# Performance work log

Measured on AMD Instinct MI355X. Metric: run time of the kernel, lower is better.

## Reference

```python
import jax, jax.numpy as jnp
import numpy as np

N_NODES = 50000


def gcn_conv(x, W, b, src, dst, n):
    """PyG GCNConv: add self-loops, symmetric deg^-1/2 normalization, then aggregate."""
    loop = jnp.arange(n, dtype=src.dtype)
    s = jnp.concatenate([src, loop])  # [E+N]
    d = jnp.concatenate([dst, loop])  # [E+N]
    deg = jax.ops.segment_sum(jnp.ones_like(d, dtype=x.dtype), d, num_segments=n)  # [N]
    dinv = jnp.where(deg > 0, jax.lax.rsqrt(deg), 0.0)
    h = x @ W  # transform first (reduces message width), [N, out]
    norm = (dinv[s] * dinv[d])[:, None]  # [E+N, 1]
    msgs = h[s] * norm  # gather + scale, [E+N, out]
    out = jax.ops.segment_sum(msgs, d, num_segments=n)  # scatter-add, [N, out]
    return out + b


def setup_inputs() -> dict:
    key = jax.random.key(0)
    k1, k2, k3, k4 = jax.random.split(key, 4)
    in_dim, hidden, n_cls = 512, 256, 64
    x = jax.random.normal(k1, (N_NODES, in_dim), dtype=jnp.float32)
    edge_index = jax.random.randint(k2, (2, 800000), 0, N_NODES, dtype=jnp.int64)
    W1 = jax.random.normal(k3, (in_dim, hidden), dtype=jnp.float32) / np.sqrt(in_dim)
    b1 = jnp.zeros((hidden,), dtype=jnp.float32)
    W2 = jax.random.normal(k4, (hidden, n_cls), dtype=jnp.float32) / np.sqrt(hidden)
    b2 = jnp.zeros((n_cls,), dtype=jnp.float32)
    return {"x": x, "edge_index": edge_index, "W1": W1, "b1": b1, "W2": W2, "b2": b2}


def reference(x, edge_index, W1, b1, W2, b2):
    src, dst = edge_index[0], edge_index[1]
    n = x.shape[0]
    h = jax.nn.relu(gcn_conv(x, W1, b1, src, dst, n))  # dropout is identity in eval mode
    logits = gcn_conv(h, W2, b2, src, dst, n)
    evidence = jax.nn.softplus(logits)
    return (evidence, h)
```

## Files before the change

### kernel.cpp

```cpp
#include <hip/hip_runtime.h>


#define N_NODES 50000
#define IN_DIM 512
#define HID 256
#define NCLS 64

typedef unsigned short u16;
typedef unsigned int u32;
typedef __attribute__((ext_vector_type(8))) short short8;
typedef __attribute__((ext_vector_type(4))) float float4_t;

__device__ __forceinline__ float bf_lo(u32 v) {
    u32 u = v << 16; float f; __builtin_memcpy(&f, &u, 4); return f;
}
__device__ __forceinline__ float bf_hi(u32 v) {
    u32 u = v & 0xffff0000u; float f; __builtin_memcpy(&f, &u, 4); return f;
}
__device__ __forceinline__ u16 f2bf(float f) {
    u32 u; __builtin_memcpy(&u, &f, 4);
    return (u16)((u + 0x7fffu + ((u >> 16) & 1u)) >> 16);
}
__device__ __forceinline__ void acc8(float* acc, uint4 v, float w) {
    acc[0] += w * bf_lo(v.x); acc[1] += w * bf_hi(v.x);
    acc[2] += w * bf_lo(v.y); acc[3] += w * bf_hi(v.y);
    acc[4] += w * bf_lo(v.z); acc[5] += w * bf_hi(v.z);
    acc[6] += w * bf_lo(v.w); acc[7] += w * bf_hi(v.w);
}

__global__ void init_kernel(int* __restrict__ cnt, int* __restrict__ cursor, int n) {
    int i = blockIdx.x * blockDim.x + threadIdx.x;
    if (i < n) { cnt[i] = 0; cursor[i] = 0; }
}

__global__ void count_kernel(const int* __restrict__ dst, int* __restrict__ cnt, int E) {
    int e = blockIdx.x * blockDim.x + threadIdx.x;
    if (e < E) atomicAdd(&cnt[dst[e]], 1);
}

__global__ __launch_bounds__(256) void s1_kernel(const int* __restrict__ cnt,
                                                 int* __restrict__ blocksum,
                                                 float* __restrict__ dinv, int n) {
    int tid = threadIdx.x;
    int i = blockIdx.x * 256 + tid;
    int c = (i < n) ? cnt[i] : 0;
    if (i < n) dinv[i] = rsqrtf((float)(c + 1));
    __shared__ int s[256];
    s[tid] = c;
    __syncthreads();
    for (int off = 128; off > 0; off >>= 1) {
        if (tid < off) s[tid] += s[tid + off];
        __syncthreads();
    }
    if (tid == 0) blocksum[blockIdx.x] = s[0];
}

__global__ __launch_bounds__(256) void s3_kernel(const int* __restrict__ cnt,
                                                 const int* __restrict__ blocksum,
                                                 int* __restrict__ row_ptr, int n, int nb) {
    __shared__ int bs[256];
    __shared__ int s[256];
    int tid = threadIdx.x;
    int v = (tid < nb) ? blocksum[tid] : 0;
    bs[tid] = v;
    __syncthreads();
    for (int off = 1; off < 256; off <<= 1) {
        int a = (tid >= off) ? bs[tid - off] : 0;
        __syncthreads();
        bs[tid] += a;
        __syncthreads();
    }
    int boff = (blockIdx.x == 0) ? 0 : bs[blockIdx.x - 1];
    int i = blockIdx.x * 256 + tid;
    int c = (i < n) ? cnt[i] : 0;
    s[tid] = c;
    __syncthreads();
    for (int off = 1; off < 256; off <<= 1) {
        int a = (tid >= off) ? s[tid - off] : 0;
        __syncthreads();
        s[tid] += a;
        __syncthreads();
    }
    if (i <= n) row_ptr[i] = boff + s[tid] - c;
}

__global__ void fill_kernel(const int* __restrict__ src, const int* __restrict__ dst,
                            const int* __restrict__ row_ptr, int* __restrict__ cursor,
                            int* __restrict__ csr_src, int E) {
    int e = blockIdx.x * blockDim.x + threadIdx.x;
    if (e >= E) return;
    int d = dst[e];
    int pos = row_ptr[d] + atomicAdd(&cursor[d], 1);
    csr_src[pos] = src[e];
}

__global__ __launch_bounds__(256) void cast_bf16_kernel(const float* __restrict__ in,
                                                        u16* __restrict__ out, int n4) {
    int i = blockIdx.x * 256 + threadIdx.x;
    if (i >= n4) return;
    float4 v = ((const float4*)in)[i];
    ushort4 o = make_ushort4(f2bf(v.x), f2bf(v.y), f2bf(v.z), f2bf(v.w));
    ((ushort4*)out)[i] = o;
}

__global__ __launch_bounds__(256) void tcast_kernel(const float* __restrict__ W,
                                                    u16* __restrict__ Wt, int K, int N) {
    int idx = blockIdx.x * 256 + threadIdx.x;
    if (idx >= K * N) return;
    int n = idx / K, k = idx - n * K;
    Wt[idx] = f2bf(W[k * N + n]);
}

template <int BM, int BN, int K, int N>
__global__ __launch_bounds__(256) void mfma_gemm_kernel(const u16* __restrict__ A,
                                                        const u16* __restrict__ Bt,
                                                        u16* __restrict__ C, int M) {
    constexpr int WCOLS = (BN >= 128) ? 2 : 1;
    constexpr int WROWS = 4 / WCOLS;
    static_assert(WROWS * 64 == BM && WCOLS * 64 == BN, "wave tiling mismatch");
    constexpr int LDSA = BM * 32;
    __shared__ u16 lds[LDSA + BN * 32];

    const int tid = threadIdx.x;
    const int wave = tid >> 6, lane = tid & 63;
    const int wm = wave / WCOLS, wn = wave % WCOLS;
    const int quad = lane >> 4, l15 = lane & 15;
    const int row0 = blockIdx.y * BM;
    const int col0 = blockIdx.x * BN;

    float4_t acc[4][4];
#pragma unroll
    for (int mi = 0; mi < 4; mi++)
#pragma unroll
        for (int ni = 0; ni < 4; ni++) {
            float4_t z = {0.f, 0.f, 0.f, 0.f};
            acc[mi][ni] = z;
        }

    for (int k0 = 0; k0 < K; k0 += 32) {
#pragma unroll
        for (int i = 0; i < BM / 64; i++) {
            int c = tid + i * 256;
            int r = c >> 2;
            int gr = row0 + r;
            gr = gr < M ? gr : M - 1;
            const u16* gp = A + (long)gr * K + k0 + (c & 3) * 8;
            u16* lp = lds + c * 8;
            __builtin_amdgcn_global_load_lds((const __attribute__((address_space(1))) u32*)gp,
                                             (__attribute__((address_space(3))) u32*)lp,
                                             16, 0, 0);
        }
#pragma unroll
        for (int i = 0; i < BN / 64; i++) {
            int c = tid + i * 256;
            int r = c >> 2;
            const u16* gp = Bt + (long)(col0 + r) * K + k0 + (c & 3) * 8;
            u16* lp = lds + LDSA + c * 8;
            __builtin_amdgcn_global_load_lds((const __attribute__((address_space(1))) u32*)gp,
                                             (__attribute__((address_space(3))) u32*)lp,
                                             16, 0, 0);
        }
        __syncthreads();

        short8 af[4], bfr[4];
#pragma unroll
        for (int mi = 0; mi < 4; mi++)
            af[mi] = *(const short8*)(lds + (wm * 64 + mi * 16 + l15) * 32 + quad * 8);
#pragma unroll
        for (int ni = 0; ni < 4; ni++)
            bfr[ni] = *(const short8*)(lds + LDSA + (wn * 64 + ni * 16 + l15) * 32 + quad * 8);
#pragma unroll
        for (int mi = 0; mi < 4; mi++)
#pragma unroll
            for (int ni = 0; ni < 4; ni++)
                acc[mi][ni] = __builtin_amdgcn_mfma_f32_16x16x32_bf16(af[mi], bfr[ni],
                                                                      acc[mi][ni], 0, 0, 0);
        __syncthreads();
    }

#pragma unroll
    for (int mi = 0; mi < 4; mi++) {
#pragma unroll
        for (int r = 0; r < 4; r++) {
            int row = row0 + wm * 64 + mi * 16 + quad * 4 + r;
            if (row < M) {
#pragma unroll
                for (int ni = 0; ni < 4; ni++) {
                    int col = col0 + wn * 64 + ni * 16 + l15;
                    C[(long)row * N + col] = f2bf(acc[mi][ni][r]);
                }
            }
        }
    }
}

__global__ __launch_bounds__(256) void agg_wide_kernel(const u16* __restrict__ t,
                                                       const int* __restrict__ row_ptr,
                                                       const int* __restrict__ csr_src,
                                                       const float* __restrict__ dinv,
                                                       const float* __restrict__ bias,
                                                       float* __restrict__ out_f,
                                                       u16* __restrict__ out_bf, int n) {
    constexpr int FEAT = 256;
    int node = (blockIdx.x * blockDim.x + threadIdx.x) >> 6;
    int lane = threadIdx.x & 63;
    if (node >= n) return;
    const int g = lane >> 5;
    const int r = lane & 31;
    float acc[8] = {};
    const int beg = row_ptr[node], end = row_ptr[node + 1];
    int e = beg;
    for (; e + 16 <= end; e += 16) {
        int s[8]; float w[8]; uint4 v[8];
#pragma unroll
        for (int u = 0; u < 8; u++) s[u] = csr_src[e + u * 2 + g];
#pragma unroll
        for (int u = 0; u < 8; u++) w[u] = dinv[s[u]];
#pragma unroll
        for (int u = 0; u < 8; u++) v[u] = *(const uint4*)(t + (long)s[u] * FEAT + r * 8);
#pragma unroll
        for (int u = 0; u < 8; u++) acc8(acc, v[u], w[u]);
    }
    for (; e + 8 <= end; e += 8) {
        int s[4]; float w[4]; uint4 v[4];
#pragma unroll
        for (int u = 0; u < 4; u++) s[u] = csr_src[e + u * 2 + g];
#pragma unroll
        for (int u = 0; u < 4; u++) w[u] = dinv[s[u]];
#pragma unroll
        for (int u = 0; u < 4; u++) v[u] = *(const uint4*)(t + (long)s[u] * FEAT + r * 8);
#pragma unroll
        for (int u = 0; u < 4; u++) acc8(acc, v[u], w[u]);
    }
    for (; e < end; e += 2) {
        int ee = e + g;
        if (ee < end) {
            int s = csr_src[ee];
            float w = dinv[s];
            uint4 v = *(const uint4*)(t + (long)s * FEAT + r * 8);
            acc8(acc, v, w);
        }
    }
#pragma unroll
    for (int j = 0; j < 8; j++) acc[j] += __shfl_xor(acc[j], 32, 64);

    if (lane < 32) {
        const float di = dinv[node];
        uint4 sv = *(const uint4*)(t + (long)node * FEAT + lane * 8);
        float self[8] = {bf_lo(sv.x), bf_hi(sv.x), bf_lo(sv.y), bf_hi(sv.y),
                         bf_lo(sv.z), bf_hi(sv.z), bf_lo(sv.w), bf_hi(sv.w)};
        float4 b0 = *(const float4*)(bias + lane * 8);
        float4 b1 = *(const float4*)(bias + lane * 8 + 4);
        float bb[8] = {b0.x, b0.y, b0.z, b0.w, b1.x, b1.y, b1.z, b1.w};
        float rv[8];
#pragma unroll
        for (int j = 0; j < 8; j++)
            rv[j] = fmaxf(di * (acc[j] + di * self[j]) + bb[j], 0.f);
        long base = (long)node * FEAT + lane * 8;
        *(float4*)(out_f + base) = make_float4(rv[0], rv[1], rv[2], rv[3]);
        *(float4*)(out_f + base + 4) = make_float4(rv[4], rv[5], rv[6], rv[7]);
        uint4 o;
        o.x = (u32)f2bf(rv[0]) | ((u32)f2bf(rv[1]) << 16);
        o.y = (u32)f2bf(rv[2]) | ((u32)f2bf(rv[3]) << 16);
        o.z = (u32)f2bf(rv[4]) | ((u32)f2bf(rv[5]) << 16);
        o.w = (u32)f2bf(rv[6]) | ((u32)f2bf(rv[7]) << 16);
        *(uint4*)(out_bf + base) = o;
    }
}

__global__ __launch_bounds__(256) void agg_n8_kernel(const u16* __restrict__ t,
                                                     const int* __restrict__ row_ptr,
                                                     const int* __restrict__ csr_src,
                                                     const float* __restrict__ dinv,
                                                     const float* __restrict__ bias,
                                                     float* __restrict__ out_f, int n) {
    constexpr int FEAT = 64;
    const int wid = (blockIdx.x * blockDim.x + threadIdx.x) >> 6;
    const int lane = threadIdx.x & 63;
    const int g = lane >> 3;
    const int r = lane & 7;
    const int node = wid * 8 + g;
    const bool valid = node < n;
    const int nd = valid ? node : (n - 1);
    const int beg = row_ptr[nd];
    const int deg = valid ? (row_ptr[nd + 1] - beg) : 0;
    float acc[8] = {};
    for (int e = 0;; e += 4) {
        if (!__any(e < deg)) break;
        int s[4]; float w[4]; uint4 v[4];
#pragma unroll
        for (int u = 0; u < 4; u++) {
            bool a = (e + u) < deg;
            s[u] = a ? csr_src[beg + e + u] : 0;
            w[u] = a ? 0.f : 0.f;
            w[u] = a ? 1.f : 0.f;
        }
#pragma unroll
        for (int u = 0; u < 4; u++) w[u] = w[u] * dinv[s[u]];
#pragma unroll
        for (int u = 0; u < 4; u++) v[u] = *(const uint4*)(t + (long)s[u] * FEAT + r * 8);
#pragma unroll
        for (int u = 0; u < 4; u++) acc8(acc, v[u], w[u]);
    }
    const float di = dinv[nd];
    uint4 sv = *(const uint4*)(t + (long)nd * FEAT + r * 8);
    float self[8] = {bf_lo(sv.x), bf_hi(sv.x), bf_lo(sv.y), bf_hi(sv.y),
                     bf_lo(sv.z), bf_hi(sv.z), bf_lo(sv.w), bf_hi(sv.w)};
    float4 b0 = *(const float4*)(bias + r * 8);
    float4 b1 = *(const float4*)(bias + r * 8 + 4);
    float bb[8] = {b0.x, b0.y, b0.z, b0.w, b1.x, b1.y, b1.z, b1.w};
    float rv[8];
#pragma unroll
    for (int j = 0; j < 8; j++) {
        float v = di * (acc[j] + di * self[j]) + bb[j];
        rv[j] = fmaxf(v, 0.f) + __logf(1.f + __expf(-fabsf(v)));
    }
    if (valid) {
        long base = (long)nd * FEAT + r * 8;
        *(float4*)(out_f + base) = make_float4(rv[0], rv[1], rv[2], rv[3]);
        *(float4*)(out_f + base + 4) = make_float4(rv[4], rv[5], rv[6], rv[7]);
    }
}

extern "C" void kernel_launch(void* const* d_in, const int* in_sizes, int n_in,
                              void* d_out, int out_size, void* d_ws, size_t ws_size,
                              hipStream_t stream) {
    const float* x  = (const float*)d_in[0];
    const int*   ei = (const int*)d_in[1];
    const float* W1 = (const float*)d_in[2];
    const float* b1 = (const float*)d_in[3];
    const float* W2 = (const float*)d_in[4];
    const float* b2 = (const float*)d_in[5];

    float* evidence = (float*)d_out;
    float* h        = (float*)d_out + (long)N_NODES * NCLS;

    const int E = in_sizes[1] / 2;
    const int* src = ei;
    const int* dst = ei + E;

    const int NB = (N_NODES + 255) / 256;

    char* w = (char*)d_ws;
    int*   cnt      = (int*)w;  w += 50048 * 4;
    int*   cursor   = (int*)w;  w += 50048 * 4;
    int*   row_ptr  = (int*)w;  w += 50064 * 4;
    float* dinv     = (float*)w; w += 50048 * 4;
    int*   blocksum = (int*)w;  w += 256 * 4;
    int*   csr_src  = (int*)w;  w += 800000 * 4;
    u16*   xbf      = (u16*)w;  w += (long)N_NODES * IN_DIM * 2;
    u16*   w1t      = (u16*)w;  w += IN_DIM * HID * 2;
    u16*   w2t      = (u16*)w;  w += HID * NCLS * 2;
    u16*   t1bf     = (u16*)w;  w += (long)N_NODES * HID * 2;
    u16*   hbf      = xbf;
    u16*   t2bf     = t1bf;

    init_kernel<<<NB, 256, 0, stream>>>(cnt, cursor, N_NODES);
    count_kernel<<<(E + 255) / 256, 256, 0, stream>>>(dst, cnt, E);
    s1_kernel<<<NB, 256, 0, stream>>>(cnt, blocksum, dinv, N_NODES);
    s3_kernel<<<NB, 256, 0, stream>>>(cnt, blocksum, row_ptr, N_NODES, NB);
    fill_kernel<<<(E + 255) / 256, 256, 0, stream>>>(src, dst, row_ptr, cursor, csr_src, E);

    cast_bf16_kernel<<<(N_NODES * IN_DIM / 4 + 255) / 256, 256, 0, stream>>>(
        x, xbf, N_NODES * IN_DIM / 4);
    tcast_kernel<<<(IN_DIM * HID + 255) / 256, 256, 0, stream>>>(W1, w1t, IN_DIM, HID);
    tcast_kernel<<<(HID * NCLS + 255) / 256, 256, 0, stream>>>(W2, w2t, HID, NCLS);

    {
        dim3 grid(HID / 128, (N_NODES + 127) / 128);
        mfma_gemm_kernel<128, 128, IN_DIM, HID><<<grid, 256, 0, stream>>>(xbf, w1t, t1bf, N_NODES);
    }
    agg_wide_kernel<<<(N_NODES * 64 + 255) / 256, 256, 0, stream>>>(
        t1bf, row_ptr, csr_src, dinv, b1, h, hbf, N_NODES);

    {
        dim3 grid(NCLS / 64, (N_NODES + 255) / 256);
        mfma_gemm_kernel<256, 64, HID, NCLS><<<grid, 256, 0, stream>>>(hbf, w2t, t2bf, N_NODES);
    }
    {
        int waves = (N_NODES + 7) / 8;
        int blocks = (waves + 3) / 4;
        agg_n8_kernel<<<blocks, 256, 0, stream>>>(
            t2bf, row_ptr, csr_src, dinv, b2, evidence, N_NODES);
    }
}
```

Before: 410.7 us.

## Fuse fp32-to-bf16 cast into GEMM A-load and prescale rows by dinv

Drops the separate x-to-bf16 cast kernel; the first GEMM now reads fp32 x directly and converts it to bf16 while staging into LDS. Both GEMMs multiply output rows by dinv in the epilogue, so the aggregation kernels no longer gather dinv per neighbour and just sum the rows. This avoids writing and re-reading a bf16 copy of x and removes one random gather per edge. In exchange, the first GEMM reads twice the bytes through a register path instead of the direct global-to-LDS load, and dinv is applied before the bf16 rounding.

```diff
diff --git a/kernel.cpp b/kernel.cpp
--- a/kernel.cpp
+++ b/kernel.cpp
@@ -20,6 +20,12 @@
 __device__ __forceinline__ u16 f2bf(float f) {
     u32 u; __builtin_memcpy(&u, &f, 4);
     return (u16)((u + 0x7fffu + ((u >> 16) & 1u)) >> 16);
+}
+__device__ __forceinline__ void add8(float* acc, uint4 v) {
+    acc[0] += bf_lo(v.x); acc[1] += bf_hi(v.x);
+    acc[2] += bf_lo(v.y); acc[3] += bf_hi(v.y);
+    acc[4] += bf_lo(v.z); acc[5] += bf_hi(v.z);
+    acc[6] += bf_lo(v.w); acc[7] += bf_hi(v.w);
 }
 __device__ __forceinline__ void acc8(float* acc, uint4 v, float w) {
     acc[0] += w * bf_lo(v.x); acc[1] += w * bf_hi(v.x);
@@ -94,15 +100,6 @@
     csr_src[pos] = src[e];
 }
 
-__global__ __launch_bounds__(256) void cast_bf16_kernel(const float* __restrict__ in,
-                                                        u16* __restrict__ out, int n4) {
-    int i = blockIdx.x * 256 + threadIdx.x;
-    if (i >= n4) return;
-    float4 v = ((const float4*)in)[i];
-    ushort4 o = make_ushort4(f2bf(v.x), f2bf(v.y), f2bf(v.z), f2bf(v.w));
-    ((ushort4*)out)[i] = o;
-}
-
 __global__ __launch_bounds__(256) void tcast_kernel(const float* __restrict__ W,
                                                     u16* __restrict__ Wt, int K, int N) {
     int idx = blockIdx.x * 256 + threadIdx.x;
@@ -111,10 +108,11 @@
     Wt[idx] = f2bf(W[k * N + n]);
 }
 
-template <int BM, int BN, int K, int N>
-__global__ __launch_bounds__(256) void mfma_gemm_kernel(const u16* __restrict__ A,
+template <int BM, int BN, int K, int N, bool AF32, bool SCALE>
+__global__ __launch_bounds__(256) void mfma_gemm_kernel(const void* __restrict__ Ain,
                                                         const u16* __restrict__ Bt,
-                                                        u16* __restrict__ C, int M) {
+                                                        u16* __restrict__ C, int M,
+                                                        const float* __restrict__ rowscale) {
     constexpr int WCOLS = (BN >= 128) ? 2 : 1;
     constexpr int WROWS = 4 / WCOLS;
     static_assert(WROWS * 64 == BM && WCOLS * 64 == BN, "wave tiling mismatch");
@@ -144,11 +142,23 @@
             int r = c >> 2;
             int gr = row0 + r;
             gr = gr < M ? gr : M - 1;
-            const u16* gp = A + (long)gr * K + k0 + (c & 3) * 8;
-            u16* lp = lds + c * 8;
-            __builtin_amdgcn_global_load_lds((const __attribute__((address_space(1))) u32*)gp,
-                                             (__attribute__((address_space(3))) u32*)lp,
-                                             16, 0, 0);
+            if constexpr (AF32) {
+                const float* gp = (const float*)Ain + (long)gr * K + k0 + (c & 3) * 8;
+                float4 p0 = ((const float4*)gp)[0];
+                float4 p1 = ((const float4*)gp)[1];
+                uint4 o;
+                o.x = (u32)f2bf(p0.x) | ((u32)f2bf(p0.y) << 16);
+                o.y = (u32)f2bf(p0.z) | ((u32)f2bf(p0.w) << 16);
+                o.z = (u32)f2bf(p1.x) | ((u32)f2bf(p1.y) << 16);
+                o.w = (u32)f2bf(p1.z) | ((u32)f2bf(p1.w) << 16);
+                *(uint4*)(lds + c * 8) = o;
+            } else {
+                const u16* gp = (const u16*)Ain + (long)gr * K + k0 + (c & 3) * 8;
+                u16* lp = lds + c * 8;
+                __builtin_amdgcn_global_load_lds((const __attribute__((address_space(1))) u32*)gp,
+                                                 (__attribute__((address_space(3))) u32*)lp,
+                                                 16, 0, 0);
+            }
         }
 #pragma unroll
         for (int i = 0; i < BN / 64; i++) {
@@ -184,10 +194,12 @@
         for (int r = 0; r < 4; r++) {
             int row = row0 + wm * 64 + mi * 16 + quad * 4 + r;
             if (row < M) {
+                float sc = 1.f;
+                if constexpr (SCALE) sc = rowscale[row];
 #pragma unroll
                 for (int ni = 0; ni < 4; ni++) {
                     int col = col0 + wn * 64 + ni * 16 + l15;
-                    C[(long)row * N + col] = f2bf(acc[mi][ni][r]);
+                    C[(long)row * N + col] = f2bf(acc[mi][ni][r] * sc);
                 }
             }
         }
@@ -211,34 +223,29 @@
     const int beg = row_ptr[node], end = row_ptr[node + 1];
     int e = beg;
     for (; e + 16 <= end; e += 16) {
-        int s[8]; float w[8]; uint4 v[8];
+        int s[8]; uint4 v[8];
 #pragma unroll
         for (int u = 0; u < 8; u++) s[u] = csr_src[e + u * 2 + g];
 #pragma unroll
-        for (int u = 0; u < 8; u++) w[u] = dinv[s[u]];
-#pragma unroll
         for (int u = 0; u < 8; u++) v[u] = *(const uint4*)(t + (long)s[u] * FEAT + r * 8);
 #pragma unroll
-        for (int u = 0; u < 8; u++) acc8(acc, v[u], w[u]);
+        for (int u = 0; u < 8; u++) add8(acc, v[u]);
     }
     for (; e + 8 <= end; e += 8) {
-        int s[4]; float w[4]; uint4 v[4];
+        int s[4]; uint4 v[4];
 #pragma unroll
         for (int u = 0; u < 4; u++) s[u] = csr_src[e + u * 2 + g];
 #pragma unroll
-        for (int u = 0; u < 4; u++) w[u] = dinv[s[u]];
-#pragma unroll
         for (int u = 0; u < 4; u++) v[u] = *(const uint4*)(t + (long)s[u] * FEAT + r * 8);
 #pragma unroll
-        for (int u = 0; u < 4; u++) acc8(acc, v[u], w[u]);
+        for (int u = 0; u < 4; u++) add8(acc, v[u]);
     }
     for (; e < end; e += 2) {
         int ee = e + g;
         if (ee < end) {
             int s = csr_src[ee];
-            float w = dinv[s];
             uint4 v = *(const uint4*)(t + (long)s * FEAT + r * 8);
-            acc8(acc, v, w);
+            add8(acc, v);
         }
     }
 #pragma unroll
@@ -255,7 +262,7 @@
         float rv[8];
 #pragma unroll
         for (int j = 0; j < 8; j++)
-            rv[j] = fmaxf(di * (acc[j] + di * self[j]) + bb[j], 0.f);
+            rv[j] = fmaxf(di * (acc[j] + self[j]) + bb[j], 0.f);
         long base = (long)node * FEAT + lane * 8;
         *(float4*)(out_f + base) = make_float4(rv[0], rv[1], rv[2], rv[3]);
         *(float4*)(out_f + base + 4) = make_float4(rv[4], rv[5], rv[6], rv[7]);
@@ -292,11 +299,8 @@
         for (int u = 0; u < 4; u++) {
             bool a = (e + u) < deg;
             s[u] = a ? csr_src[beg + e + u] : 0;
-            w[u] = a ? 0.f : 0.f;
             w[u] = a ? 1.f : 0.f;
         }
-#pragma unroll
-        for (int u = 0; u < 4; u++) w[u] = w[u] * dinv[s[u]];
 #pragma unroll
         for (int u = 0; u < 4; u++) v[u] = *(const uint4*)(t + (long)s[u] * FEAT + r * 8);
 #pragma unroll
@@ -312,7 +316,7 @@
     float rv[8];
 #pragma unroll
     for (int j = 0; j < 8; j++) {
-        float v = di * (acc[j] + di * self[j]) + bb[j];
+        float v = di * (acc[j] + self[j]) + bb[j];
         rv[j] = fmaxf(v, 0.f) + __logf(1.f + __expf(-fabsf(v)));
     }
     if (valid) {
@@ -348,11 +352,10 @@
     float* dinv     = (float*)w; w += 50048 * 4;
     int*   blocksum = (int*)w;  w += 256 * 4;
     int*   csr_src  = (int*)w;  w += 800000 * 4;
-    u16*   xbf      = (u16*)w;  w += (long)N_NODES * IN_DIM * 2;
+    u16*   hbf      = (u16*)w;  w += (long)N_NODES * IN_DIM * 2;
     u16*   w1t      = (u16*)w;  w += IN_DIM * HID * 2;
     u16*   w2t      = (u16*)w;  w += HID * NCLS * 2;
     u16*   t1bf     = (u16*)w;  w += (long)N_NODES * HID * 2;
-    u16*   hbf      = xbf;
     u16*   t2bf     = t1bf;
 
     init_kernel<<<NB, 256, 0, stream>>>(cnt, cursor, N_NODES);
@@ -361,21 +364,21 @@
     s3_kernel<<<NB, 256, 0, stream>>>(cnt, blocksum, row_ptr, N_NODES, NB);
     fill_kernel<<<(E + 255) / 256, 256, 0, stream>>>(src, dst, row_ptr, cursor, csr_src, E);
 
-    cast_bf16_kernel<<<(N_NODES * IN_DIM / 4 + 255) / 256, 256, 0, stream>>>(
-        x, xbf, N_NODES * IN_DIM / 4);
     tcast_kernel<<<(IN_DIM * HID + 255) / 256, 256, 0, stream>>>(W1, w1t, IN_DIM, HID);
     tcast_kernel<<<(HID * NCLS + 255) / 256, 256, 0, stream>>>(W2, w2t, HID, NCLS);
 
     {
         dim3 grid(HID / 128, (N_NODES + 127) / 128);
-        mfma_gemm_kernel<128, 128, IN_DIM, HID><<<grid, 256, 0, stream>>>(xbf, w1t, t1bf, N_NODES);
+        mfma_gemm_kernel<128, 128, IN_DIM, HID, true, true>
+            <<<grid, 256, 0, stream>>>(x, w1t, t1bf, N_NODES, dinv);
     }
     agg_wide_kernel<<<(N_NODES * 64 + 255) / 256, 256, 0, stream>>>(
         t1bf, row_ptr, csr_src, dinv, b1, h, hbf, N_NODES);
 
     {
         dim3 grid(NCLS / 64, (N_NODES + 255) / 256);
-        mfma_gemm_kernel<256, 64, HID, NCLS><<<grid, 256, 0, stream>>>(hbf, w2t, t2bf, N_NODES);
+        mfma_gemm_kernel<256, 64, HID, NCLS, false, true>
+            <<<grid, 256, 0, stream>>>(hbf, w2t, t2bf, N_NODES, dinv);
     }
     {
         int waves = (N_NODES + 7) / 8;
```

Measured after the change: 406.6 us. Within noise of the previous version (-1.0%).
